# Kernel optimization log

Measured on AMD Instinct MI355X. Metric: run time of the kernel, lower is better.

## Reference

```python
import jax, jax.numpy as jnp
import numpy as np

NUM_HEADS = 8
EMBED = 512
HEAD_DIM = EMBED // NUM_HEADS
B, S = 4, 2048


def setup_inputs() -> dict:
    key = jax.random.key(0)
    ks = jax.random.split(key, 8)
    sc = 0.02
    return {
        "values": jax.random.normal(ks[0], (B, S, EMBED), dtype=jnp.float32),
        "keys": jax.random.normal(ks[1], (B, S, EMBED), dtype=jnp.float32),
        "query": jax.random.normal(ks[2], (B, S, EMBED), dtype=jnp.float32),
        "Wv": jax.random.normal(ks[3], (HEAD_DIM, HEAD_DIM), dtype=jnp.float32) * sc,
        "Wk": jax.random.normal(ks[4], (HEAD_DIM, HEAD_DIM), dtype=jnp.float32) * sc,
        "Wq": jax.random.normal(ks[5], (HEAD_DIM, HEAD_DIM), dtype=jnp.float32) * sc,
        "Wo": jax.random.normal(ks[6], (EMBED, EMBED), dtype=jnp.float32) * sc,
        "bo": jnp.zeros((EMBED,), dtype=jnp.float32),
    }


def reference(values, keys, query, Wv, Wk, Wq, Wo, bo):
    b, s, _ = query.shape
    # split heads: [B, S, H, D]
    v = values.reshape(b, s, NUM_HEADS, HEAD_DIM)
    k = keys.reshape(b, s, NUM_HEADS, HEAD_DIM)
    q = query.reshape(b, s, NUM_HEADS, HEAD_DIM)
    # per-head linear (nn.Linear: x @ W.T), weights shared across heads
    v = jnp.einsum("bshd,ed->bshe", v, Wv)
    k = jnp.einsum("bshd,ed->bshe", k, Wk)
    q = jnp.einsum("bshd,ed->bshe", q, Wq)
    # energy: [B, H, Q, K]
    energy = jnp.einsum("bqhd,bkhd->bhqk", q, k)
    # NOTE: original scales by sqrt(embed_size), not sqrt(head_dim)
    attn = jax.nn.softmax(energy / jnp.sqrt(jnp.float32(EMBED)), axis=-1)
    out = jnp.einsum("bhqk,bkhd->bqhd", attn, v).reshape(b, s, EMBED)
    return out @ Wo.T + bo
```

## Files before the change

### kernel.cpp

```cpp
#include <hip/hip_runtime.h>

#define H 8
#define D 64
#define E 512
#define BATCH 4
#define SEQ 2048

typedef __bf16 bf16v8 __attribute__((ext_vector_type(8)));
typedef float f32v4 __attribute__((ext_vector_type(4)));
typedef unsigned int u32v4 __attribute__((ext_vector_type(4)));
typedef unsigned short u16v4 __attribute__((ext_vector_type(4)));

#define MFMA16(a,b,c) __builtin_amdgcn_mfma_f32_16x16x32_bf16(a,b,c,0,0,0)

#define AS1 __attribute__((address_space(1)))
#define AS3 __attribute__((address_space(3)))
#define GLDS16(g, l) __builtin_amdgcn_global_load_lds((const AS1 void*)(g), (AS3 void*)(l), 16, 0, 0)

static __device__ __forceinline__ unsigned short f2bf(float f) {
  unsigned u = __builtin_bit_cast(unsigned, f);
  u += 0x7fffu + ((u >> 16) & 1u);
  return (unsigned short)(u >> 16);
}

static __device__ __forceinline__ float exp2_hw(float x) {
#if __has_builtin(__builtin_amdgcn_exp2f)
  return __builtin_amdgcn_exp2f(x);
#else
  return exp2f(x);
#endif
}

static __device__ __forceinline__ bf16v8 lds16(const char* p) {
  return __builtin_bit_cast(bf16v8, *(const u32v4*)p);
}

__global__ void prep_all(const float* __restrict__ Wo, const float* __restrict__ Wv,
                         const float* __restrict__ Wq, const float* __restrict__ Wk,
                         const float* __restrict__ v, const float* __restrict__ keys,
                         unsigned short* __restrict__ Wo2, unsigned short* __restrict__ MT,
                         unsigned short* __restrict__ vT, unsigned short* __restrict__ kb) {
  __shared__ float tile[64][65];
  int bx = blockIdx.x;
  int t = threadIdx.x;
  if (bx < 1024) {
    int i = bx * 256 + t;
    int n = i >> 9, c = i & 511;
    int h = c >> 6, d = c & 63;
    float acc = 0.f;
    for (int e = 0; e < 64; ++e) acc += Wo[n*512 + h*64 + e] * Wv[e*64 + d];
    Wo2[n*512 + c] = f2bf(acc);
  } else if (bx < 1040) {
    int i = (bx - 1024) * 256 + t;
    int d2 = i >> 6, d1 = i & 63;
    float acc = 0.f;
    for (int e = 0; e < 64; ++e) acc += Wq[e*64 + d1] * Wk[e*64 + d2];
    MT[d2*64 + d1] = f2bf(acc * 0.04419417382415922f);
  } else {
    int flat = bx - 1040;
    int bh = flat >> 5, sc = flat & 31;
    int b = bh >> 3, h = bh & 7;
    {
      const float* kp = keys + (size_t)flat * 4096;
      unsigned short* ko = kb + (size_t)flat * 4096;
      #pragma unroll
      for (int i = 0; i < 4; ++i) {
        f32v4 x = *(const f32v4*)(kp + (i*256 + t)*4);
        u16v4 o = { f2bf(x[0]), f2bf(x[1]), f2bf(x[2]), f2bf(x[3]) };
        *(u16v4*)(ko + (i*256 + t)*4) = o;
      }
    }
    #pragma unroll
    for (int i = 0; i < 16; ++i) {
      int idx = i*256 + t; int si = idx >> 6, d = idx & 63;
      tile[si][d] = v[((size_t)(b*SEQ + sc*64 + si))*E + h*64 + d];
    }
    __syncthreads();
    #pragma unroll
    for (int i = 0; i < 16; ++i) {
      int idx = i*256 + t; int d = idx >> 6, si = idx & 63;
      vT[((size_t)(bh*64 + d))*SEQ + sc*64 + si] = f2bf(tile[si][d]);
    }
  }
}

__global__ __launch_bounds__(256, 2) void attn(const float* __restrict__ query,
                                               const unsigned short* __restrict__ MT,
                                               const unsigned short* __restrict__ kb,
                                               const unsigned short* __restrict__ vT,
                                               unsigned short* __restrict__ ao) {
  __shared__ __align__(16) char lds[49152];
  int bh = blockIdx.y, b = bh >> 3, h = bh & 7;
  int qt = blockIdx.x;
  int tid = threadIdx.x, w = tid >> 6, lane = tid & 63, hi = lane >> 4, lo = lane & 15;
  char* pw = lds + 32768 + w*4096;

  const unsigned short* kbase = kb + (size_t)(b*SEQ)*E + h*64;
  const unsigned short* vbase = vT + (size_t)bh*64*SEQ;
  int srow = tid >> 3, scc = tid & 7;

  #pragma unroll
  for (int i = 0; i < 2; ++i) {
    int row = i*32 + srow;
    int sc = scc ^ (row & 7);
    GLDS16(kbase + (size_t)row*E + sc*8,   lds        + i*4096 + w*1024);
    GLDS16(vbase + (size_t)row*SEQ + sc*8, lds + 8192 + i*4096 + w*1024);
  }
  {
    char* xl = lds + 16384;
    char* ml = lds + 32768;
    #pragma unroll
    for (int i = 0; i < 8; ++i) {
      int c = i*256 + tid;
      int row = c >> 4, cc = c & 15;
      f32v4 xv = *(const f32v4*)(query + (size_t)(b*SEQ + qt*128 + row)*E + h*64 + cc*4);
      u16v4 o = { f2bf(xv[0]), f2bf(xv[1]), f2bf(xv[2]), f2bf(xv[3]) };
      int off = row*128 + ((((cc >> 1) ^ (row & 7))) << 4) + (cc & 1)*8;
      *(u16v4*)(xl + off) = o;
    }
    #pragma unroll
    for (int i = 0; i < 2; ++i) {
      int c = i*256 + tid; int row = c >> 3, cc = c & 7;
      *(u32v4*)(ml + row*128 + ((cc ^ (row & 7)) << 4)) = *(const u32v4*)(MT + row*64 + cc*8);
    }
  }
  __syncthreads();

  bf16v8 qa[2][2];
  {
    char* xl = lds + 16384;
    char* ml = lds + 32768;
    f32v4 qacc[2][4] = {};
    #pragma unroll
    for (int kk = 0; kk < 2; ++kk)
      #pragma unroll
      for (int mrep = 0; mrep < 2; ++mrep) {
        int arow = w*32 + mrep*16 + lo;
        bf16v8 af = lds16(xl + arow*128 + (((kk*4 + hi) ^ (arow & 7)) << 4));
        #pragma unroll
        for (int nt = 0; nt < 4; ++nt) {
          int brow = nt*16 + lo;
          bf16v8 bf_ = lds16(ml + brow*128 + (((kk*4 + hi) ^ (brow & 7)) << 4));
          qacc[mrep][nt] = MFMA16(af, bf_, qacc[mrep][nt]);
        }
      }
    __syncthreads();
    #pragma unroll
    for (int mrep = 0; mrep < 2; ++mrep)
      #pragma unroll
      for (int nt = 0; nt < 4; ++nt)
        #pragma unroll
        for (int r = 0; r < 4; ++r) {
          int qrw = mrep*16 + 4*hi + r;
          *(unsigned short*)(pw + qrw*128 + ((nt*32 + lo*2) ^ ((qrw & 7) << 4))) =
              f2bf(qacc[mrep][nt][r]);
        }
    asm volatile("s_waitcnt lgkmcnt(0)" ::: "memory");
    __builtin_amdgcn_sched_barrier(0);
    #pragma unroll
    for (int mrep = 0; mrep < 2; ++mrep)
      #pragma unroll
      for (int kk = 0; kk < 2; ++kk) {
        int row = mrep*16 + lo;
        qa[mrep][kk] = lds16(pw + row*128 + (((kk*4 + hi) ^ (lo & 7)) << 4));
      }
  }

  f32v4 oacc[2][4] = {};
  float lsum[2][4] = {};

  for (int kt = 0; kt < 32; ++kt) {
    const char* klc = lds + (kt & 1)*16384;
    const char* vlc = klc + 8192;
    if (kt < 31) {
      char* kln = lds + ((kt & 1) ^ 1)*16384;
      #pragma unroll
      for (int i = 0; i < 2; ++i) {
        int row = i*32 + srow;
        int sc = scc ^ (row & 7);
        GLDS16(kbase + (size_t)((kt+1)*64 + row)*E + sc*8, kln        + i*4096 + w*1024);
        GLDS16(vbase + (size_t)row*SEQ + (kt+1)*64 + sc*8, kln + 8192 + i*4096 + w*1024);
      }
    }
    f32v4 sacc[2][4] = {};
    __builtin_amdgcn_s_setprio(1);
    #pragma unroll
    for (int nt = 0; nt < 4; ++nt)
      #pragma unroll
      for (int kk = 0; kk < 2; ++kk) {
        int row = nt*16 + lo;
        bf16v8 kf = lds16(klc + row*128 + (((kk*4 + hi) ^ (row & 7)) << 4));
        sacc[0][nt] = MFMA16(qa[0][kk], kf, sacc[0][nt]);
        sacc[1][nt] = MFMA16(qa[1][kk], kf, sacc[1][nt]);
      }
    __builtin_amdgcn_s_setprio(0);
    #pragma unroll
    for (int mrep = 0; mrep < 2; ++mrep)
      #pragma unroll
      for (int nt = 0; nt < 4; ++nt)
        #pragma unroll
        for (int r = 0; r < 4; ++r) {
          float p = exp2_hw(sacc[mrep][nt][r] * 1.4426950408889634f);
          lsum[mrep][r] += p;
          int qrw = mrep*16 + 4*hi + r;
          *(unsigned short*)(pw + qrw*128 + ((nt*32 + lo*2) ^ ((qrw & 7) << 4))) = f2bf(p);
        }
    asm volatile("s_waitcnt lgkmcnt(0)" ::: "memory");
    __builtin_amdgcn_sched_barrier(0);
    __builtin_amdgcn_s_setprio(1);
    #pragma unroll
    for (int ks = 0; ks < 2; ++ks) {
      bf16v8 pa0 = lds16(pw + lo*128        + (((ks*4 + hi) ^ (lo & 7)) << 4));
      bf16v8 pa1 = lds16(pw + (16+lo)*128   + (((ks*4 + hi) ^ (lo & 7)) << 4));
      #pragma unroll
      for (int dt = 0; dt < 4; ++dt) {
        int row = dt*16 + lo;
        bf16v8 vf = lds16(vlc + row*128 + (((ks*4 + hi) ^ (row & 7)) << 4));
        oacc[0][dt] = MFMA16(pa0, vf, oacc[0][dt]);
        oacc[1][dt] = MFMA16(pa1, vf, oacc[1][dt]);
      }
    }
    __builtin_amdgcn_s_setprio(0);
    __syncthreads();
  }
  #pragma unroll
  for (int mrep = 0; mrep < 2; ++mrep)
    #pragma unroll
    for (int r = 0; r < 4; ++r) {
      #pragma unroll
      for (int m = 1; m < 16; m <<= 1) lsum[mrep][r] += __shfl_xor(lsum[mrep][r], m, 64);
      lsum[mrep][r] = __builtin_amdgcn_rcpf(lsum[mrep][r]);
    }
  #pragma unroll
  for (int mrep = 0; mrep < 2; ++mrep)
    #pragma unroll
    for (int dt = 0; dt < 4; ++dt)
      #pragma unroll
      for (int r = 0; r < 4; ++r) {
        int tok = b*SEQ + qt*128 + w*32 + mrep*16 + 4*hi + r;
        ao[(size_t)tok*E + h*64 + dt*16 + lo] = f2bf(oacc[mrep][dt][r] * lsum[mrep][r]);
      }
}

__global__ __launch_bounds__(256, 2) void final_gemm(const unsigned short* __restrict__ ao,
                                                     const unsigned short* __restrict__ wo2,
                                                     const float* __restrict__ bo,
                                                     float* __restrict__ out) {
  __shared__ __align__(16) char lds[65536];
  int m0 = blockIdx.x * 128, n0 = blockIdx.y * 128;
  int tid = threadIdx.x, w = tid >> 6, lane = tid & 63, hi = lane >> 4, lo = lane & 15;
  int wm = (w >> 1) * 64, wn = (w & 1) * 64;
  int srow = tid >> 3, scc = tid & 7;
  f32v4 acc[4][4] = {};
  #pragma unroll
  for (int i = 0; i < 4; ++i) {
    int row = i*32 + srow;
    int sc = scc ^ (row & 7);
    GLDS16(ao  + (size_t)(m0 + row)*E + sc*8, lds         + i*4096 + w*1024);
    GLDS16(wo2 + (size_t)(n0 + row)*E + sc*8, lds + 16384 + i*4096 + w*1024);
  }
  __syncthreads();
  for (int kt = 0; kt < 8; ++kt) {
    const char* al = lds + (kt & 1)*32768;
    const char* bl = al + 16384;
    if (kt < 7) {
      char* an = lds + ((kt & 1) ^ 1)*32768;
      #pragma unroll
      for (int i = 0; i < 4; ++i) {
        int row = i*32 + srow;
        int sc = scc ^ (row & 7);
        GLDS16(ao  + (size_t)(m0 + row)*E + (kt+1)*64 + sc*8, an         + i*4096 + w*1024);
        GLDS16(wo2 + (size_t)(n0 + row)*E + (kt+1)*64 + sc*8, an + 16384 + i*4096 + w*1024);
      }
    }
    __builtin_amdgcn_s_setprio(1);
    #pragma unroll
    for (int kk = 0; kk < 2; ++kk) {
      bf16v8 af[4], bfv[4];
      #pragma unroll
      for (int mt = 0; mt < 4; ++mt) {
        int row = wm + mt*16 + lo;
        af[mt] = lds16(al + row*128 + (((kk*4 + hi) ^ (row & 7)) << 4));
      }
      #pragma unroll
      for (int nt = 0; nt < 4; ++nt) {
        int row = wn + nt*16 + lo;
        bfv[nt] = lds16(bl + row*128 + (((kk*4 + hi) ^ (row & 7)) << 4));
      }
      #pragma unroll
      for (int mt = 0; mt < 4; ++mt)
        #pragma unroll
        for (int nt = 0; nt < 4; ++nt)
          acc[mt][nt] = MFMA16(af[mt], bfv[nt], acc[mt][nt]);
    }
    __builtin_amdgcn_s_setprio(0);
    __syncthreads();
  }
  #pragma unroll
  for (int nt = 0; nt < 4; ++nt) {
    float bias = bo[n0 + wn + nt*16 + lo];
    #pragma unroll
    for (int mt = 0; mt < 4; ++mt)
      #pragma unroll
      for (int r = 0; r < 4; ++r)
        out[(size_t)(m0 + wm + mt*16 + 4*hi + r)*E + n0 + wn + nt*16 + lo] =
            acc[mt][nt][r] + bias;
  }
}

extern "C" void kernel_launch(void* const* d_in, const int* in_sizes, int n_in,
                              void* d_out, int out_size, void* d_ws, size_t ws_size,
                              hipStream_t stream) {
  const float* values = (const float*)d_in[0];
  const float* keys   = (const float*)d_in[1];
  const float* query  = (const float*)d_in[2];
  const float* Wv     = (const float*)d_in[3];
  const float* Wk     = (const float*)d_in[4];
  const float* Wq     = (const float*)d_in[5];
  const float* Wo     = (const float*)d_in[6];
  const float* bo     = (const float*)d_in[7];
  float* out = (float*)d_out;
  char* ws = (char*)d_ws;

  unsigned short* MT  = (unsigned short*)(ws);
  unsigned short* Wo2 = (unsigned short*)(ws + 8192);
  unsigned short* kb  = (unsigned short*)(ws + (1u  << 20));
  unsigned short* vT  = (unsigned short*)(ws + (9u  << 20));
  unsigned short* ao  = (unsigned short*)(ws + (17u << 20));

  prep_all  <<<2064, 256, 0, stream>>>(Wo, Wv, Wq, Wk, values, keys, Wo2, MT, vT, kb);
  attn      <<<dim3(16, 32), 256, 0, stream>>>(query, MT, kb, vT, ao);
  final_gemm<<<dim3(64, 4),  256, 0, stream>>>(ao, Wo2, bo, out);
}
```

Baseline: 171.4 us.

## Keep softmax probabilities in registers via transposed MFMA and lane permutes

```diff
diff --git a/kernel.cpp b/kernel.cpp
--- a/kernel.cpp
+++ b/kernel.cpp
@@ -33,6 +33,12 @@
 
 static __device__ __forceinline__ bf16v8 lds16(const char* p) {
   return __builtin_bit_cast(bf16v8, *(const u32v4*)p);
+}
+
+static __device__ __forceinline__ unsigned cvtpk(float a, float b) {
+  unsigned r;
+  asm("v_cvt_pk_bf16_f32 %0, %1, %2" : "=v"(r) : "v"(a), "v"(b));
+  return r;
 }
 
 __global__ void prep_all(const float* __restrict__ Wo, const float* __restrict__ Wv,
@@ -89,11 +95,11 @@
                                                const unsigned short* __restrict__ kb,
                                                const unsigned short* __restrict__ vT,
                                                unsigned short* __restrict__ ao) {
-  __shared__ __align__(16) char lds[49152];
+  __shared__ __align__(16) char lds[40960];
   int bh = blockIdx.y, b = bh >> 3, h = bh & 7;
   int qt = blockIdx.x;
   int tid = threadIdx.x, w = tid >> 6, lane = tid & 63, hi = lane >> 4, lo = lane & 15;
-  char* pw = lds + 32768 + w*4096;
+  int b4 = hi & 1;
 
   const unsigned short* kbase = kb + (size_t)(b*SEQ)*E + h*64;
   const unsigned short* vbase = vT + (size_t)bh*64*SEQ;
@@ -130,6 +136,7 @@
   {
     char* xl = lds + 16384;
     char* ml = lds + 32768;
+    char* sq = lds + 16384 + w*4096;
     f32v4 qacc[2][4] = {};
     #pragma unroll
     for (int kk = 0; kk < 2; ++kk)
@@ -144,7 +151,6 @@
           qacc[mrep][nt] = MFMA16(af, bf_, qacc[mrep][nt]);
         }
       }
-    __syncthreads();
     #pragma unroll
     for (int mrep = 0; mrep < 2; ++mrep)
       #pragma unroll
@@ -152,7 +158,7 @@
         #pragma unroll
         for (int r = 0; r < 4; ++r) {
           int qrw = mrep*16 + 4*hi + r;
-          *(unsigned short*)(pw + qrw*128 + ((nt*32 + lo*2) ^ ((qrw & 7) << 4))) =
+          *(unsigned short*)(sq + qrw*128 + ((nt*32 + lo*2) ^ ((qrw & 7) << 4))) =
               f2bf(qacc[mrep][nt][r]);
         }
     asm volatile("s_waitcnt lgkmcnt(0)" ::: "memory");
@@ -162,12 +168,13 @@
       #pragma unroll
       for (int kk = 0; kk < 2; ++kk) {
         int row = mrep*16 + lo;
-        qa[mrep][kk] = lds16(pw + row*128 + (((kk*4 + hi) ^ (lo & 7)) << 4));
-      }
-  }
+        qa[mrep][kk] = lds16(sq + row*128 + (((kk*4 + hi) ^ (lo & 7)) << 4));
+      }
+  }
+  __syncthreads();
 
   f32v4 oacc[2][4] = {};
-  float lsum[2][4] = {};
+  float lsum[2] = {0.f, 0.f};
 
   for (int kt = 0; kt < 32; ++kt) {
     const char* klc = lds + (kt & 1)*16384;
@@ -190,56 +197,78 @@
       for (int kk = 0; kk < 2; ++kk) {
         int row = nt*16 + lo;
         bf16v8 kf = lds16(klc + row*128 + (((kk*4 + hi) ^ (row & 7)) << 4));
-        sacc[0][nt] = MFMA16(qa[0][kk], kf, sacc[0][nt]);
-        sacc[1][nt] = MFMA16(qa[1][kk], kf, sacc[1][nt]);
+        sacc[0][nt] = MFMA16(kf, qa[0][kk], sacc[0][nt]);
+        sacc[1][nt] = MFMA16(kf, qa[1][kk], sacc[1][nt]);
       }
     __builtin_amdgcn_s_setprio(0);
-    #pragma unroll
-    for (int mrep = 0; mrep < 2; ++mrep)
-      #pragma unroll
-      for (int nt = 0; nt < 4; ++nt)
-        #pragma unroll
-        for (int r = 0; r < 4; ++r) {
-          float p = exp2_hw(sacc[mrep][nt][r] * 1.4426950408889634f);
-          lsum[mrep][r] += p;
-          int qrw = mrep*16 + 4*hi + r;
-          *(unsigned short*)(pw + qrw*128 + ((nt*32 + lo*2) ^ ((qrw & 7) << 4))) = f2bf(p);
+    unsigned wv[2][2][2][2];
+    #pragma unroll
+    for (int m = 0; m < 2; ++m)
+      #pragma unroll
+      for (int nt = 0; nt < 4; ++nt) {
+        float p0 = exp2_hw(sacc[m][nt][0] * 1.4426950408889634f);
+        float p1 = exp2_hw(sacc[m][nt][1] * 1.4426950408889634f);
+        float p2 = exp2_hw(sacc[m][nt][2] * 1.4426950408889634f);
+        float p3 = exp2_hw(sacc[m][nt][3] * 1.4426950408889634f);
+        lsum[m] += (p0 + p1) + (p2 + p3);
+        wv[m][nt >> 1][nt & 1][0] = cvtpk(p0, p1);
+        wv[m][nt >> 1][nt & 1][1] = cvtpk(p2, p3);
+      }
+    #pragma unroll
+    for (int m = 0; m < 2; ++m)
+      #pragma unroll
+      for (int nt1 = 0; nt1 < 2; ++nt1)
+        #pragma unroll
+        for (int s = 0; s < 2; ++s)
+          asm("v_permlane32_swap_b32 %0, %1"
+              : "+v"(wv[m][nt1][0][s]), "+v"(wv[m][nt1][1][s]));
+    #pragma unroll
+    for (int m = 0; m < 2; ++m)
+      #pragma unroll
+      for (int nt1 = 0; nt1 < 2; ++nt1)
+        #pragma unroll
+        for (int s = 0; s < 2; ++s) {
+          int sent = b4 ? (int)wv[m][nt1][0][s] : (int)wv[m][nt1][1][s];
+          unsigned recv = (unsigned)__shfl_xor(sent, 16);
+          unsigned n0 = b4 ? recv : wv[m][nt1][0][s];
+          unsigned n1 = b4 ? wv[m][nt1][1][s] : recv;
+          wv[m][nt1][0][s] = n0;
+          wv[m][nt1][1][s] = n1;
         }
-    asm volatile("s_waitcnt lgkmcnt(0)" ::: "memory");
-    __builtin_amdgcn_sched_barrier(0);
     __builtin_amdgcn_s_setprio(1);
     #pragma unroll
     for (int ks = 0; ks < 2; ++ks) {
-      bf16v8 pa0 = lds16(pw + lo*128        + (((ks*4 + hi) ^ (lo & 7)) << 4));
-      bf16v8 pa1 = lds16(pw + (16+lo)*128   + (((ks*4 + hi) ^ (lo & 7)) << 4));
+      u32v4 c0 = { wv[0][ks][0][0], wv[0][ks][0][1], wv[0][ks][1][0], wv[0][ks][1][1] };
+      u32v4 c1 = { wv[1][ks][0][0], wv[1][ks][0][1], wv[1][ks][1][0], wv[1][ks][1][1] };
+      bf16v8 pb0 = __builtin_bit_cast(bf16v8, c0);
+      bf16v8 pb1 = __builtin_bit_cast(bf16v8, c1);
       #pragma unroll
       for (int dt = 0; dt < 4; ++dt) {
         int row = dt*16 + lo;
         bf16v8 vf = lds16(vlc + row*128 + (((ks*4 + hi) ^ (row & 7)) << 4));
-        oacc[0][dt] = MFMA16(pa0, vf, oacc[0][dt]);
-        oacc[1][dt] = MFMA16(pa1, vf, oacc[1][dt]);
+        oacc[0][dt] = MFMA16(vf, pb0, oacc[0][dt]);
+        oacc[1][dt] = MFMA16(vf, pb1, oacc[1][dt]);
       }
     }
     __builtin_amdgcn_s_setprio(0);
     __syncthreads();
   }
   #pragma unroll
-  for (int mrep = 0; mrep < 2; ++mrep)
-    #pragma unroll
-    for (int r = 0; r < 4; ++r) {
-      #pragma unroll
-      for (int m = 1; m < 16; m <<= 1) lsum[mrep][r] += __shfl_xor(lsum[mrep][r], m, 64);
-      lsum[mrep][r] = __builtin_amdgcn_rcpf(lsum[mrep][r]);
-    }
-  #pragma unroll
-  for (int mrep = 0; mrep < 2; ++mrep)
-    #pragma unroll
-    for (int dt = 0; dt < 4; ++dt)
-      #pragma unroll
-      for (int r = 0; r < 4; ++r) {
-        int tok = b*SEQ + qt*128 + w*32 + mrep*16 + 4*hi + r;
-        ao[(size_t)tok*E + h*64 + dt*16 + lo] = f2bf(oacc[mrep][dt][r] * lsum[mrep][r]);
-      }
+  for (int m = 0; m < 2; ++m) {
+    lsum[m] += __shfl_xor(lsum[m], 16);
+    lsum[m] += __shfl_xor(lsum[m], 32);
+    lsum[m] = __builtin_amdgcn_rcpf(lsum[m]);
+  }
+  #pragma unroll
+  for (int m = 0; m < 2; ++m) {
+    int tok = b*SEQ + qt*128 + w*32 + m*16 + lo;
+    #pragma unroll
+    for (int dt = 0; dt < 4; ++dt) {
+      u16v4 o = { f2bf(oacc[m][dt][0] * lsum[m]), f2bf(oacc[m][dt][1] * lsum[m]),
+                  f2bf(oacc[m][dt][2] * lsum[m]), f2bf(oacc[m][dt][3] * lsum[m]) };
+      *(u16v4*)(ao + (size_t)tok*E + h*64 + dt*16 + 4*hi) = o;
+    }
+  }
 }
 
 __global__ __launch_bounds__(256, 2) void final_gemm(const unsigned short* __restrict__ ao,
```

New measurement: 163.9 us. -4.4%, faster.
